# Kernel optimization log

Hardware: AMD Instinct MI355X
Metric: run time of the kernel (lower is better)

The kernel has to match this reference:

```python
import jax, jax.numpy as jnp
import numpy as np

WS = 8          # window side -> N = 64
DIM = 512
NH = 16
B_ = 1024       # batch * num_windows
CPB_HIDDEN = 512


def _make_coords_table():
    # relative_coords_table: (1, 2*WS-1, 2*WS-1, 2), log-spaced continuous coords
    r = np.arange(-(WS - 1), WS, dtype=np.float32)
    t = np.stack(np.meshgrid(r, r, indexing='ij'), axis=-1)[None]  # (1,15,15,2)
    t = t / (WS - 1)
    t = t * 8.0
    t = np.sign(t) * np.log2(np.abs(t) + 1.0) / np.log2(8.0)
    return t.astype(np.float32)


def _make_rel_pos_index():
    coords = np.stack(np.meshgrid(np.arange(WS), np.arange(WS), indexing='ij'))  # (2,WS,WS)
    cf = coords.reshape(2, -1)                       # (2, N)
    rel = (cf[:, :, None] - cf[:, None, :]).transpose(1, 2, 0).astype(np.int64)  # (N,N,2)
    rel[..., 0] += WS - 1
    rel[..., 1] += WS - 1
    rel[..., 0] *= 2 * WS - 1
    return rel.sum(-1)  # (N, N) int


def setup_inputs() -> dict:
    key = jax.random.key(0)
    ks = jax.random.split(key, 10)
    s_in = 1.0 / np.sqrt(DIM)
    inp = {
        'x': jax.random.normal(ks[0], (B_, WS * WS, DIM), dtype=jnp.float32),
        'qkv_weight': jax.random.normal(ks[1], (3 * DIM, DIM), dtype=jnp.float32) * s_in,
        'q_bias': jnp.zeros((DIM,), dtype=jnp.float32),
        'v_bias': jnp.zeros((DIM,), dtype=jnp.float32),
        'logit_scale': jnp.full((NH, 1, 1), np.log(10.0), dtype=jnp.float32),
        'cpb_w1': jax.random.normal(ks[2], (CPB_HIDDEN, 2), dtype=jnp.float32) * (1.0 / np.sqrt(2.0)),
        'cpb_b1': jnp.zeros((CPB_HIDDEN,), dtype=jnp.float32),
        'cpb_w2': jax.random.normal(ks[3], (NH, CPB_HIDDEN), dtype=jnp.float32) * (1.0 / np.sqrt(CPB_HIDDEN)),
        'proj_w': jax.random.normal(ks[4], (DIM, DIM), dtype=jnp.float32) * s_in,
        'proj_b': jnp.zeros((DIM,), dtype=jnp.float32),
        'rel_coords_table': jnp.asarray(_make_coords_table()),
        'rel_pos_index': jnp.asarray(_make_rel_pos_index()),
    }
    return inp


def reference(x, qkv_weight, q_bias, v_bias, logit_scale, cpb_w1, cpb_b1, cpb_w2,
              proj_w, proj_b, rel_coords_table, rel_pos_index):
    B, N, C = x.shape
    nh = logit_scale.shape[0]
    hd = C // nh

    # qkv projection; bias = [q_bias, 0, v_bias] (k has no bias, Swin-V2 style)
    qkv_bias = jnp.concatenate([q_bias, jnp.zeros_like(q_bias), v_bias])
    qkv = x @ qkv_weight.T + qkv_bias                       # (B, N, 3C)
    qkv = qkv.reshape(B, N, 3, nh, hd).transpose(2, 0, 3, 1, 4)  # (3, B, nh, N, hd)
    q, k, v = qkv[0], qkv[1], qkv[2]

    # continuous position bias MLP: Linear(2,512)+ReLU -> Linear(512,nh, no bias)
    hidden = jax.nn.relu(rel_coords_table @ cpb_w1.T + cpb_b1)  # (1,15,15,512)
    table = (hidden @ cpb_w2.T).reshape(-1, nh)                 # ((2W-1)^2, nh)
    rpb = table[rel_pos_index.reshape(-1)].reshape(N, N, nh).transpose(2, 0, 1)
    rpb = 16.0 * jax.nn.sigmoid(rpb)                            # (nh, N, N)

    # fused attention math: (QK^T)*logit_scale + bias -> softmax -> AV
    scores = jnp.einsum('bhnd,bhmd->bhnm', q, k) * logit_scale.reshape(1, nh, 1, 1)
    scores = scores + rpb[None]
    attn = jax.nn.softmax(scores, axis=-1)
    out = jnp.einsum('bhnm,bhmd->bhnd', attn, v)                # (B, nh, N, hd)
    out = out.transpose(0, 2, 1, 3).reshape(B, N, C)

    return out @ proj_w.T + proj_b
```

## Files before the change

### kernel.cpp

```cpp
#include <hip/hip_runtime.h>
#include <hip/hip_bf16.h>
#include <stdint.h>
#include <stddef.h>


typedef unsigned short ushort_t;
typedef _Float16 half_t;
typedef __attribute__((ext_vector_type(8))) _Float16 half8;
typedef __attribute__((ext_vector_type(4))) float f32x4;

#define MROWS 65536

__device__ __forceinline__ ushort_t h_bits(half_t h) {
  union { half_t h; ushort_t u; } c; c.h = h; return c.u;
}

__device__ __forceinline__ void gload16(const void* g, void* l) {
  __builtin_amdgcn_global_load_lds(
      (const __attribute__((address_space(1))) unsigned int*)g,
      (__attribute__((address_space(3))) unsigned int*)l, 16, 0, 0);
}

__global__ __launch_bounds__(256) void k_split(const float* __restrict__ src,
                                               ushort_t* __restrict__ hi,
                                               ushort_t* __restrict__ lo, int n4) {
  int stride = gridDim.x * blockDim.x;
  for (int i = blockIdx.x * blockDim.x + threadIdx.x; i < n4; i += stride) {
    f32x4 x = reinterpret_cast<const f32x4*>(src)[i];
    ushort_t h4[4], l4[4];
#pragma unroll
    for (int j = 0; j < 4; ++j) {
      half_t hh = (half_t)x[j];
      h4[j] = h_bits(hh);
      l4[j] = h_bits((half_t)(x[j] - (float)hh));
    }
    reinterpret_cast<uint2*>(hi)[i] =
        make_uint2(h4[0] | ((unsigned)h4[1] << 16), h4[2] | ((unsigned)h4[3] << 16));
    reinterpret_cast<uint2*>(lo)[i] =
        make_uint2(l4[0] | ((unsigned)l4[1] << 16), l4[2] | ((unsigned)l4[3] << 16));
  }
}

__global__ __launch_bounds__(256) void k_split_h(const float* __restrict__ src,
                                                 ushort_t* __restrict__ hi, int n4) {
  int stride = gridDim.x * blockDim.x;
  for (int i = blockIdx.x * blockDim.x + threadIdx.x; i < n4; i += stride) {
    f32x4 x = reinterpret_cast<const f32x4*>(src)[i];
    ushort_t h4[4];
#pragma unroll
    for (int j = 0; j < 4; ++j) h4[j] = h_bits((half_t)x[j]);
    reinterpret_cast<uint2*>(hi)[i] =
        make_uint2(h4[0] | ((unsigned)h4[1] << 16), h4[2] | ((unsigned)h4[3] << 16));
  }
}

__global__ __launch_bounds__(256) void k_cpb1(const float* __restrict__ coords,
                                              const float* __restrict__ w1,
                                              const float* __restrict__ b1,
                                              const float* __restrict__ w2,
                                              float* __restrict__ tbl) {
  __shared__ float hid[512];
  int p = blockIdx.x;
  float c0 = coords[2 * p], c1 = coords[2 * p + 1];
  int t = threadIdx.x;
  for (int j = t; j < 512; j += 256) {
    float v = c0 * w1[2 * j] + c1 * w1[2 * j + 1] + b1[j];
    hid[j] = v > 0.f ? v : 0.f;
  }
  __syncthreads();
  int wid = t >> 6, lane = t & 63;
#pragma unroll
  for (int hh = 0; hh < 4; ++hh) {
    int head = wid * 4 + hh;
    float s = 0.f;
    for (int j = lane; j < 512; j += 64) s += hid[j] * w2[head * 512 + j];
#pragma unroll
    for (int off = 32; off > 0; off >>= 1) s += __shfl_xor(s, off);
    if (lane == 0) tbl[p * 16 + head] = 16.f / (1.f + __expf(-s));
  }
}

__global__ __launch_bounds__(256) void k_cpb2(const float* __restrict__ tbl,
                                              const int* __restrict__ ridx,
                                              float* __restrict__ rpb) {
  int idx = blockIdx.x * 256 + threadIdx.x;
  int h = idx >> 12, nm = idx & 4095;
  rpb[idx] = tbl[ridx[nm] * 16 + h];
}

__device__ __forceinline__ int swz(int c, int r) {
  return c ^ (r & 3) ^ ((r >> 2) & 3);
}

__global__ __launch_bounds__(256, 4) void k_qkv(
    const ushort_t* __restrict__ Wh, const ushort_t* __restrict__ Wl,
    const float* __restrict__ X,
    const float* __restrict__ qb, const float* __restrict__ vb,
    ushort_t* __restrict__ oqh, ushort_t* __restrict__ oql,
    ushort_t* __restrict__ okh, ushort_t* __restrict__ okl,
    ushort_t* __restrict__ ovt) {
  __shared__ ushort_t lA[2][4096];
  __shared__ ushort_t lB[2][4096];

  int nwg = gridDim.x, bid = blockIdx.x;
  int idx = ((nwg & 7) == 0) ? ((bid & 7) * (nwg >> 3) + (bid >> 3)) : bid;
  int tm = idx % 12, tn = idx / 12;
  int tid = threadIdx.x;
  int wid = tid >> 6, lane = tid & 63;
  int wr = wid >> 1, wc = wid & 1;
  int lr = lane & 15, lq = lane >> 4;

  int rA = tid >> 2, qA = tid & 3;
  size_t gA = (size_t)(tm * 128 + rA) * 512 + (swz(qA, rA) << 3);
  int dA = wid * 512;

  int rB = tid >> 3, qB = tid & 7;
  const float* gB = X + (size_t)(tn * 128 + rB) * 512 + qB * 4;
  int dB = rB * 32 + (swz(qB >> 1, rB) << 3) + ((qB & 1) << 2);

  f32x4 acc[4][4];
#pragma unroll
  for (int i = 0; i < 4; ++i)
#pragma unroll
    for (int j = 0; j < 4; ++j)
#pragma unroll
      for (int r = 0; r < 4; ++r) acc[i][j][r] = 0.f;

  auto stageA = [&](int t2, int bs) {
    int kk = (t2 & 15) * 32;
    const ushort_t* W = (t2 >= 16) ? Wl : Wh;
    gload16(W + gA + kk, &lA[bs][dA]);
    gload16(W + gA + 32768 + kk, &lA[bs][2048 + dA]);
  };
  auto loadB = [&](int t2, f32x4* xr) {
    int kk = (t2 & 15) * 32;
#pragma unroll
    for (int s = 0; s < 4; ++s) xr[s] = *(const f32x4*)(gB + s * 16384 + kk);
  };
  auto writeB = [&](const f32x4* xr, int bs) {
#pragma unroll
    for (int s = 0; s < 4; ++s) {
      ushort_t h4[4];
#pragma unroll
      for (int e = 0; e < 4; ++e) h4[e] = h_bits((half_t)xr[s][e]);
      *(uint2*)&lB[bs][dB + s * 1024] =
          make_uint2(h4[0] | ((unsigned)h4[1] << 16), h4[2] | ((unsigned)h4[3] << 16));
    }
  };

  f32x4 xr[4];
  stageA(0, 0);
  loadB(0, xr);
  writeB(xr, 0);
  const int c16 = swz(lq, lr) << 3;
#pragma unroll 2
  for (int t = 0; t < 32; ++t) {
    __syncthreads();
    int bs = t & 1;
    if (t < 31) {
      stageA(t + 1, bs ^ 1);
      loadB(t + 1, xr);
    }
    half8 af[4], bf[4];
#pragma unroll
    for (int i = 0; i < 4; ++i)
      af[i] = *(const half8*)&lA[bs][(wr * 64 + i * 16 + lr) * 32 + c16];
#pragma unroll
    for (int j = 0; j < 4; ++j)
      bf[j] = *(const half8*)&lB[bs][(wc * 64 + j * 16 + lr) * 32 + c16];
    __builtin_amdgcn_s_setprio(1);
#pragma unroll
    for (int i = 0; i < 4; ++i)
#pragma unroll
      for (int j = 0; j < 4; ++j)
        acc[i][j] = __builtin_amdgcn_mfma_f32_16x16x32_f16(af[i], bf[j], acc[i][j], 0, 0, 0);
    __builtin_amdgcn_s_setprio(0);
    if (t < 31) writeB(xr, bs ^ 1);
  }

#pragma unroll
  for (int i = 0; i < 4; ++i) {
    int ch0 = tm * 128 + wr * 64 + i * 16 + lq * 4;
#pragma unroll
    for (int j = 0; j < 4; ++j) {
      int tok = tn * 128 + wc * 64 + j * 16 + lr;
      int sec = tm >> 2;
      int h = (ch0 >> 5) & 15, d0 = ch0 & 31;
      int win = tok >> 6, n = tok & 63;
      size_t pr = (size_t)win * 16 + h;
      f32x4 b4;
      if (sec == 0)      b4 = *(const f32x4*)&qb[ch0];
      else if (sec == 2) b4 = *(const f32x4*)&vb[ch0 - 1024];
      else { b4[0] = 0.f; b4[1] = 0.f; b4[2] = 0.f; b4[3] = 0.f; }
      if (sec == 2) {
#pragma unroll
        for (int r = 0; r < 4; ++r) {
          float v = acc[i][j][r] + b4[r];
          ovt[(pr * 32 + d0 + r) * 64 + n] = h_bits((half_t)v);
        }
      } else {
        ushort_t hb[4], lb4[4];
#pragma unroll
        for (int r = 0; r < 4; ++r) {
          float v = acc[i][j][r] + b4[r];
          half_t hh = (half_t)v;
          hb[r] = h_bits(hh);
          lb4[r] = h_bits((half_t)(v - (float)hh));
        }
        uint2 hw = make_uint2(hb[0] | ((unsigned)hb[1] << 16), hb[2] | ((unsigned)hb[3] << 16));
        uint2 lw = make_uint2(lb4[0] | ((unsigned)lb4[1] << 16), lb4[2] | ((unsigned)lb4[3] << 16));
        size_t o = (pr * 64 + n) * 32 + d0;
        if (sec == 0) { *(uint2*)&oqh[o] = hw; *(uint2*)&oql[o] = lw; }
        else          { *(uint2*)&okh[o] = hw; *(uint2*)&okl[o] = lw; }
      }
    }
  }
}

__global__ __launch_bounds__(256, 4) void k_proj(
    const ushort_t* __restrict__ Wh,
    const ushort_t* __restrict__ Bp,
    const float* __restrict__ pb, float* __restrict__ outp) {
  __shared__ ushort_t lA[2][4096];
  __shared__ ushort_t lB[2][4096];

  int nwg = gridDim.x, bid = blockIdx.x;
  int idx = ((nwg & 7) == 0) ? ((bid & 7) * (nwg >> 3) + (bid >> 3)) : bid;
  int tm = idx % 4, tn = idx / 4;
  int tid = threadIdx.x;
  int wid = tid >> 6, lane = tid & 63;
  int wr = wid >> 1, wc = wid & 1;
  int lr = lane & 15, lq = lane >> 4;

  int rA = tid >> 2, qA = tid & 3;
  int sw = swz(qA, rA) << 3;
  size_t gA = (size_t)(tm * 128 + rA) * 512 + sw;
  size_t gB = (size_t)(tn * 128 + rA) * 512 + sw;
  int dA = wid * 512;

  f32x4 acc[4][4];
#pragma unroll
  for (int i = 0; i < 4; ++i)
#pragma unroll
    for (int j = 0; j < 4; ++j)
#pragma unroll
      for (int r = 0; r < 4; ++r) acc[i][j][r] = 0.f;

  auto stage = [&](int kk, int bs) {
    gload16(Wh + gA + kk, &lA[bs][dA]);
    gload16(Wh + gA + 32768 + kk, &lA[bs][2048 + dA]);
    gload16(Bp + gB + kk, &lB[bs][dA]);
    gload16(Bp + gB + 32768 + kk, &lB[bs][2048 + dA]);
  };

  stage(0, 0);
  const int c16 = swz(lq, lr) << 3;
#pragma unroll 2
  for (int t = 0; t < 16; ++t) {
    __syncthreads();
    int bs = t & 1;
    if (t < 15) stage((t + 1) * 32, bs ^ 1);
    half8 af[4], bf[4];
#pragma unroll
    for (int i = 0; i < 4; ++i)
      af[i] = *(const half8*)&lA[bs][(wr * 64 + i * 16 + lr) * 32 + c16];
#pragma unroll
    for (int j = 0; j < 4; ++j)
      bf[j] = *(const half8*)&lB[bs][(wc * 64 + j * 16 + lr) * 32 + c16];
    __builtin_amdgcn_s_setprio(1);
#pragma unroll
    for (int i = 0; i < 4; ++i)
#pragma unroll
      for (int j = 0; j < 4; ++j)
        acc[i][j] = __builtin_amdgcn_mfma_f32_16x16x32_f16(af[i], bf[j], acc[i][j], 0, 0, 0);
    __builtin_amdgcn_s_setprio(0);
  }

#pragma unroll
  for (int i = 0; i < 4; ++i) {
    int ch0 = tm * 128 + wr * 64 + i * 16 + lq * 4;
    f32x4 b4 = *(const f32x4*)&pb[ch0];
#pragma unroll
    for (int j = 0; j < 4; ++j) {
      int tok = tn * 128 + wc * 64 + j * 16 + lr;
      f32x4 o;
#pragma unroll
      for (int r = 0; r < 4; ++r) o[r] = acc[i][j][r] + b4[r];
      *(f32x4*)&outp[(size_t)tok * 512 + ch0] = o;
    }
  }
}

__global__ __launch_bounds__(128) void k_attn(
    const ushort_t* __restrict__ qph, const ushort_t* __restrict__ qpl,
    const ushort_t* __restrict__ kph, const ushort_t* __restrict__ kpl,
    const ushort_t* __restrict__ vt,
    const float* __restrict__ rpb, const float* __restrict__ lsc,
    ushort_t* __restrict__ oh) {
  __shared__ unsigned pw[2][2][64 * 36];
  const int tid = threadIdx.x;
  const int wid = tid >> 6, lane = tid & 63;
  const int pair = blockIdx.x * 2 + wid;
  const int h = pair & 15;
  const int l15 = lane & 15, lq = lane >> 4;
  const size_t base = (size_t)pair * 2048;

  half8 Kh[4], Kl[4], Qh[4], Ql[4];
#pragma unroll
  for (int t4 = 0; t4 < 4; ++t4) {
    int off = (t4 * 16 + l15) * 32 + lq * 8;
    Kh[t4] = *(const half8*)(kph + base + off);
    Kl[t4] = *(const half8*)(kpl + base + off);
    Qh[t4] = *(const half8*)(qph + base + off);
    Ql[t4] = *(const half8*)(qpl + base + off);
  }
  f32x4 st[4][4];
#pragma unroll
  for (int a = 0; a < 4; ++a)
#pragma unroll
    for (int b = 0; b < 4; ++b)
#pragma unroll
      for (int r = 0; r < 4; ++r) st[a][b][r] = 0.f;
#pragma unroll
  for (int kvt = 0; kvt < 4; ++kvt)
#pragma unroll
    for (int qt = 0; qt < 4; ++qt) {
      st[kvt][qt] = __builtin_amdgcn_mfma_f32_16x16x32_f16(Kh[kvt], Qh[qt], st[kvt][qt], 0, 0, 0);
      st[kvt][qt] = __builtin_amdgcn_mfma_f32_16x16x32_f16(Kh[kvt], Ql[qt], st[kvt][qt], 0, 0, 0);
      st[kvt][qt] = __builtin_amdgcn_mfma_f32_16x16x32_f16(Kl[kvt], Qh[qt], st[kvt][qt], 0, 0, 0);
    }

  const float ls = lsc[h];
  const float* rb = rpb + ((size_t)h << 12);
  float mx[4], sm[4], inv[4];
#pragma unroll
  for (int qt = 0; qt < 4; ++qt) {
    int qg = qt * 16 + l15;
    mx[qt] = -1e30f;
#pragma unroll
    for (int kvt = 0; kvt < 4; ++kvt) {
      f32x4 r4 = *(const f32x4*)(rb + qg * 64 + kvt * 16 + lq * 4);
#pragma unroll
      for (int r = 0; r < 4; ++r) {
        float z = st[kvt][qt][r] * ls + r4[r];
        st[kvt][qt][r] = z;
        mx[qt] = fmaxf(mx[qt], z);
      }
    }
    mx[qt] = fmaxf(mx[qt], __shfl_xor(mx[qt], 16));
    mx[qt] = fmaxf(mx[qt], __shfl_xor(mx[qt], 32));
    sm[qt] = 0.f;
#pragma unroll
    for (int kvt = 0; kvt < 4; ++kvt)
#pragma unroll
      for (int r = 0; r < 4; ++r) {
        float e = __expf(st[kvt][qt][r] - mx[qt]);
        st[kvt][qt][r] = e;
        sm[qt] += e;
      }
    sm[qt] += __shfl_xor(sm[qt], 16);
    sm[qt] += __shfl_xor(sm[qt], 32);
    inv[qt] = 1.f / sm[qt];
  }

#pragma unroll
  for (int qt = 0; qt < 4; ++qt) {
    int qg = qt * 16 + l15;
#pragma unroll
    for (int kvt = 0; kvt < 4; ++kvt)
#pragma unroll
      for (int p2 = 0; p2 < 2; ++p2) {
        float pa = st[kvt][qt][2 * p2] * inv[qt];
        float pc = st[kvt][qt][2 * p2 + 1] * inv[qt];
        half_t ha = (half_t)pa, hc = (half_t)pc;
        unsigned wh = h_bits(ha) | ((unsigned)h_bits(hc) << 16);
        unsigned wl = h_bits((half_t)(pa - (float)ha)) |
                      ((unsigned)h_bits((half_t)(pc - (float)hc)) << 16);
        int kv = kvt * 16 + lq * 4 + 2 * p2;
        pw[wid][0][qg * 36 + (kv >> 1)] = wh;
        pw[wid][1][qg * 36 + (kv >> 1)] = wl;
      }
  }

  half8 Vf[2][2];
#pragma unroll
  for (int dt = 0; dt < 2; ++dt)
#pragma unroll
    for (int ks = 0; ks < 2; ++ks)
      Vf[dt][ks] = *(const half8*)(vt + base + (dt * 16 + l15) * 64 + ks * 32 + lq * 8);
  f32x4 ot[2][4];
#pragma unroll
  for (int a = 0; a < 2; ++a)
#pragma unroll
    for (int b = 0; b < 4; ++b)
#pragma unroll
      for (int r = 0; r < 4; ++r) ot[a][b][r] = 0.f;
  const char* pb0 = (const char*)&pw[wid][0][0];
  const char* pb1 = (const char*)&pw[wid][1][0];
#pragma unroll
  for (int qt = 0; qt < 4; ++qt)
#pragma unroll
    for (int ks = 0; ks < 2; ++ks) {
      int off = (qt * 16 + l15) * 144 + ks * 64 + lq * 16;
      half8 Pf = *(const half8*)(pb0 + off);
      half8 Pl = *(const half8*)(pb1 + off);
#pragma unroll
      for (int dt = 0; dt < 2; ++dt) {
        ot[dt][qt] = __builtin_amdgcn_mfma_f32_16x16x32_f16(Vf[dt][ks], Pf, ot[dt][qt], 0, 0, 0);
        ot[dt][qt] = __builtin_amdgcn_mfma_f32_16x16x32_f16(Vf[dt][ks], Pl, ot[dt][qt], 0, 0, 0);
      }
    }

  int win = pair >> 4;
#pragma unroll
  for (int dt = 0; dt < 2; ++dt)
#pragma unroll
    for (int qt = 0; qt < 4; ++qt) {
      int t = win * 64 + qt * 16 + l15;
      int d0 = dt * 16 + lq * 4;
      ushort_t hb[4];
#pragma unroll
      for (int r = 0; r < 4; ++r) hb[r] = h_bits((half_t)ot[dt][qt][r]);
      *(uint2*)&oh[(size_t)t * 512 + h * 32 + d0] =
          make_uint2(hb[0] | ((unsigned)hb[1] << 16), hb[2] | ((unsigned)hb[3] << 16));
    }
}

extern "C" void kernel_launch(void* const* d_in, const int* in_sizes, int n_in,
                              void* d_out, int out_size, void* d_ws, size_t ws_size,
                              hipStream_t stream) {
  const float* x      = (const float*)d_in[0];
  const float* qkvw   = (const float*)d_in[1];
  const float* qb     = (const float*)d_in[2];
  const float* vb     = (const float*)d_in[3];
  const float* lsc    = (const float*)d_in[4];
  const float* w1     = (const float*)d_in[5];
  const float* b1     = (const float*)d_in[6];
  const float* w2     = (const float*)d_in[7];
  const float* pwt    = (const float*)d_in[8];
  const float* pb     = (const float*)d_in[9];
  const float* coords = (const float*)d_in[10];
  const int*   ridx   = (const int*)d_in[11];
  float* out = (float*)d_out;
  char* ws = (char*)d_ws;

  size_t off = 0;
  auto alloc = [&](size_t bytes) {
    size_t r = off;
    off = (off + bytes + 255) & ~(size_t)255;
    return r;
  };
  size_t oWQH = alloc((size_t)1536 * 512 * 2);
  size_t oWQL = alloc((size_t)1536 * 512 * 2);
  size_t oWPH = alloc((size_t)512 * 512 * 2);
  size_t oRPB = alloc((size_t)16 * 4096 * 4);
  size_t oTBL = alloc((size_t)225 * 16 * 4);
  size_t fixed = off;

  int S = 1;
  while (S <= 32) {
    size_t Ms = (size_t)MROWS / S;
    size_t need = fixed + Ms * 1024 * 6 + 4096;
    if (need <= ws_size) break;
    S <<= 1;
  }
  if (S > 64) S = 64;
  size_t Ms = (size_t)MROWS / S;

  size_t oQH = alloc(Ms * 1024);
  size_t oQL = alloc(Ms * 1024);
  size_t oKH = alloc(Ms * 1024);
  size_t oKL = alloc(Ms * 1024);
  size_t oVT = alloc(Ms * 1024);
  size_t oAO = alloc(Ms * 1024);

  ushort_t* wqh = (ushort_t*)(ws + oWQH);
  ushort_t* wql = (ushort_t*)(ws + oWQL);
  ushort_t* wph = (ushort_t*)(ws + oWPH);
  float* rpb = (float*)(ws + oRPB);
  float* tbl = (float*)(ws + oTBL);
  ushort_t* qh = (ushort_t*)(ws + oQH);
  ushort_t* ql = (ushort_t*)(ws + oQL);
  ushort_t* kh = (ushort_t*)(ws + oKH);
  ushort_t* kl = (ushort_t*)(ws + oKL);
  ushort_t* vt = (ushort_t*)(ws + oVT);
  ushort_t* ao = (ushort_t*)(ws + oAO);

  k_split<<<768, 256, 0, stream>>>(qkvw, wqh, wql, 1536 * 512 / 4);
  k_split_h<<<256, 256, 0, stream>>>(pwt, wph, 512 * 512 / 4);
  k_cpb1<<<225, 256, 0, stream>>>(coords, w1, b1, w2, tbl);
  k_cpb2<<<256, 256, 0, stream>>>(tbl, ridx, rpb);

  int ntn = (int)(Ms / 128);
  int g0 = 12 * ntn;
  int g1 = 4 * ntn;
  int ga = (int)((Ms / 64) * 16 / 2);

  for (int s = 0; s < S; ++s) {
    const float* xs = x + (size_t)s * Ms * 512;
    k_qkv<<<g0, 256, 0, stream>>>(wqh, wql, xs, qb, vb, qh, ql, kh, kl, vt);
    k_attn<<<ga, 128, 0, stream>>>(qh, ql, kh, kl, vt, rpb, lsc, ao);
    k_proj<<<g1, 256, 0, stream>>>(wph, ao, pb, out + (size_t)s * Ms * 512);
  }
  (void)in_sizes; (void)n_in; (void)out_size; (void)ws_size;
}
```

Before: 728.2 us.

## Pre-convert X to fp16 and load all QKV GEMM operands via LDS DMA

Adds a separate k_split_h pass that converts each X slice to fp16 in workspace, so the QKV GEMM can stage X with global_load_lds instead of fp32 register loads, conversion and LDS writes. The hi and lo weight halves are now staged together and accumulated in one 16-step K loop rather than two sequential 16-step passes over K, so each X tile is loaded once instead of twice. This costs an extra kernel launch and a round trip of the fp16 X buffer through memory per slice, more LDS per block, and occupancy reduced from 4 to 3 blocks per CU.

```diff
diff --git a/kernel.cpp b/kernel.cpp
--- a/kernel.cpp
+++ b/kernel.cpp
@@ -92,14 +92,15 @@
   return c ^ (r & 3) ^ ((r >> 2) & 3);
 }
 
-__global__ __launch_bounds__(256, 4) void k_qkv(
+__global__ __launch_bounds__(256, 3) void k_qkv(
     const ushort_t* __restrict__ Wh, const ushort_t* __restrict__ Wl,
-    const float* __restrict__ X,
+    const ushort_t* __restrict__ Xh,
     const float* __restrict__ qb, const float* __restrict__ vb,
     ushort_t* __restrict__ oqh, ushort_t* __restrict__ oql,
     ushort_t* __restrict__ okh, ushort_t* __restrict__ okl,
     ushort_t* __restrict__ ovt) {
-  __shared__ ushort_t lA[2][4096];
+  __shared__ ushort_t lAh[2][4096];
+  __shared__ ushort_t lAl[2][4096];
   __shared__ ushort_t lB[2][4096];
 
   int nwg = gridDim.x, bid = blockIdx.x;
@@ -111,13 +112,11 @@
   int lr = lane & 15, lq = lane >> 4;
 
   int rA = tid >> 2, qA = tid & 3;
-  size_t gA = (size_t)(tm * 128 + rA) * 512 + (swz(qA, rA) << 3);
+  int sw = swz(qA, rA) << 3;
+  size_t gA = (size_t)(tm * 128 + rA) * 512 + sw;
+  size_t gB = (size_t)(tn * 128 + rA) * 512 + sw;
   int dA = wid * 512;
 
-  int rB = tid >> 3, qB = tid & 7;
-  const float* gB = X + (size_t)(tn * 128 + rB) * 512 + qB * 4;
-  int dB = rB * 32 + (swz(qB >> 1, rB) << 3) + ((qB & 1) << 2);
-
   f32x4 acc[4][4];
 #pragma unroll
   for (int i = 0; i < 4; ++i)
@@ -126,45 +125,29 @@
 #pragma unroll
       for (int r = 0; r < 4; ++r) acc[i][j][r] = 0.f;
 
-  auto stageA = [&](int t2, int bs) {
-    int kk = (t2 & 15) * 32;
-    const ushort_t* W = (t2 >= 16) ? Wl : Wh;
-    gload16(W + gA + kk, &lA[bs][dA]);
-    gload16(W + gA + 32768 + kk, &lA[bs][2048 + dA]);
+  auto stage = [&](int kk, int bs) {
+    gload16(Wh + gA + kk, &lAh[bs][dA]);
+    gload16(Wh + gA + 32768 + kk, &lAh[bs][2048 + dA]);
+    gload16(Wl + gA + kk, &lAl[bs][dA]);
+    gload16(Wl + gA + 32768 + kk, &lAl[bs][2048 + dA]);
+    gload16(Xh + gB + kk, &lB[bs][dA]);
+    gload16(Xh + gB + 32768 + kk, &lB[bs][2048 + dA]);
   };
-  auto loadB = [&](int t2, f32x4* xr) {
-    int kk = (t2 & 15) * 32;
-#pragma unroll
-    for (int s = 0; s < 4; ++s) xr[s] = *(const f32x4*)(gB + s * 16384 + kk);
-  };
-  auto writeB = [&](const f32x4* xr, int bs) {
-#pragma unroll
-    for (int s = 0; s < 4; ++s) {
-      ushort_t h4[4];
-#pragma unroll
-      for (int e = 0; e < 4; ++e) h4[e] = h_bits((half_t)xr[s][e]);
-      *(uint2*)&lB[bs][dB + s * 1024] =
-          make_uint2(h4[0] | ((unsigned)h4[1] << 16), h4[2] | ((unsigned)h4[3] << 16));
-    }
-  };
-
-  f32x4 xr[4];
-  stageA(0, 0);
-  loadB(0, xr);
-  writeB(xr, 0);
+
+  stage(0, 0);
   const int c16 = swz(lq, lr) << 3;
 #pragma unroll 2
-  for (int t = 0; t < 32; ++t) {
+  for (int t = 0; t < 16; ++t) {
     __syncthreads();
     int bs = t & 1;
-    if (t < 31) {
-      stageA(t + 1, bs ^ 1);
-      loadB(t + 1, xr);
-    }
-    half8 af[4], bf[4];
-#pragma unroll
-    for (int i = 0; i < 4; ++i)
-      af[i] = *(const half8*)&lA[bs][(wr * 64 + i * 16 + lr) * 32 + c16];
+    if (t < 15) stage((t + 1) * 32, bs ^ 1);
+    half8 ah[4], al[4], bf[4];
+#pragma unroll
+    for (int i = 0; i < 4; ++i) {
+      int ro = (wr * 64 + i * 16 + lr) * 32 + c16;
+      ah[i] = *(const half8*)&lAh[bs][ro];
+      al[i] = *(const half8*)&lAl[bs][ro];
+    }
 #pragma unroll
     for (int j = 0; j < 4; ++j)
       bf[j] = *(const half8*)&lB[bs][(wc * 64 + j * 16 + lr) * 32 + c16];
@@ -172,10 +155,11 @@
 #pragma unroll
     for (int i = 0; i < 4; ++i)
 #pragma unroll
-      for (int j = 0; j < 4; ++j)
-        acc[i][j] = __builtin_amdgcn_mfma_f32_16x16x32_f16(af[i], bf[j], acc[i][j], 0, 0, 0);
+      for (int j = 0; j < 4; ++j) {
+        acc[i][j] = __builtin_amdgcn_mfma_f32_16x16x32_f16(ah[i], bf[j], acc[i][j], 0, 0, 0);
+        acc[i][j] = __builtin_amdgcn_mfma_f32_16x16x32_f16(al[i], bf[j], acc[i][j], 0, 0, 0);
+      }
     __builtin_amdgcn_s_setprio(0);
-    if (t < 31) writeB(xr, bs ^ 1);
   }
 
 #pragma unroll
@@ -460,13 +444,14 @@
   int S = 1;
   while (S <= 32) {
     size_t Ms = (size_t)MROWS / S;
-    size_t need = fixed + Ms * 1024 * 6 + 4096;
+    size_t need = fixed + Ms * 1024 * 7 + 4096;
     if (need <= ws_size) break;
     S <<= 1;
   }
   if (S > 64) S = 64;
   size_t Ms = (size_t)MROWS / S;
 
+  size_t oXH = alloc(Ms * 1024);
   size_t oQH = alloc(Ms * 1024);
   size_t oQL = alloc(Ms * 1024);
   size_t oKH = alloc(Ms * 1024);
@@ -479,6 +464,7 @@
   ushort_t* wph = (ushort_t*)(ws + oWPH);
   float* rpb = (float*)(ws + oRPB);
   float* tbl = (float*)(ws + oTBL);
+  ushort_t* xh = (ushort_t*)(ws + oXH);
   ushort_t* qh = (ushort_t*)(ws + oQH);
   ushort_t* ql = (ushort_t*)(ws + oQL);
   ushort_t* kh = (ushort_t*)(ws + oKH);
@@ -491,6 +477,9 @@
   k_cpb1<<<225, 256, 0, stream>>>(coords, w1, b1, w2, tbl);
   k_cpb2<<<256, 256, 0, stream>>>(tbl, ridx, rpb);
 
+  int n4x = (int)(Ms * 512 / 4);
+  int gsplit = (n4x + 255) / 256;
+  if (gsplit > 2048) gsplit = 2048;
   int ntn = (int)(Ms / 128);
   int g0 = 12 * ntn;
   int g1 = 4 * ntn;
@@ -498,7 +487,8 @@
 
   for (int s = 0; s < S; ++s) {
     const float* xs = x + (size_t)s * Ms * 512;
-    k_qkv<<<g0, 256, 0, stream>>>(wqh, wql, xs, qb, vb, qh, ql, kh, kl, vt);
+    k_split_h<<<gsplit, 256, 0, stream>>>(xs, xh, n4x);
+    k_qkv<<<g0, 256, 0, stream>>>(wqh, wql, xh, qb, vb, qh, ql, kh, kl, vt);
     k_attn<<<ga, 128, 0, stream>>>(qh, ql, kh, kl, vt, rpb, lsc, ao);
     k_proj<<<g1, 256, 0, stream>>>(wph, ao, pb, out + (size_t)s * Ms * 512);
   }
```

New measurement: 681.4 us. 6.4% less time.
